# Kernel optimization log

Hardware: AMD Instinct MI355X
Metric: run time of the kernel (lower is better)

Reference implementation:

```python
import jax, jax.numpy as jnp
import numpy as np

B, S, H, NH, KVH, HD = 8, 4096, 4096, 32, 8, 128
STEP = 2048
EPS = 1e-6


def _rotate_half(x):
    x1, x2 = x[..., : HD // 2], x[..., HD // 2 :]
    return jnp.concatenate([-x2, x1], axis=-1)


def _rmsnorm(x, w):
    xf = x.astype(jnp.float32)
    var = jnp.mean(xf * xf, axis=-1, keepdims=True)
    return w * (xf * jax.lax.rsqrt(var + EPS)).astype(x.dtype)


def setup_inputs() -> dict:
    key = jax.random.key(0)
    ks = jax.random.split(key, 10)
    wscale = 0.02
    hidden_states = jax.random.normal(ks[0], (B, 1, H), jnp.float32)
    # RoPE angles for position STEP
    inv_freq = 1.0 / (10000.0 ** (jnp.arange(0, HD, 2, dtype=jnp.float32) / HD))
    ang = STEP * inv_freq  # [HD/2]
    emb = jnp.concatenate([ang, ang])  # [HD]
    cos = jnp.broadcast_to(jnp.cos(emb), (B, 1, HD)).astype(jnp.float32)
    sin = jnp.broadcast_to(jnp.sin(emb), (B, 1, HD)).astype(jnp.float32)
    key_cache = jax.random.normal(ks[1], (B, KVH, S, HD), jnp.float32)
    value_cache = jax.random.normal(ks[2], (B, KVH, S, HD), jnp.float32)
    # additive causal mask: rows 0..STEP, cols 0..S-1; -1e9 where col > row
    rows = jnp.arange(STEP + 1)[:, None]
    cols = jnp.arange(S)[None, :]
    causal_mask = jnp.where(cols <= rows, 0.0, -1e9).astype(jnp.float32)[None, None]
    q_w = jax.random.normal(ks[3], (H, NH * HD), jnp.float32) * wscale
    k_w = jax.random.normal(ks[4], (H, KVH * HD), jnp.float32) * wscale
    v_w = jax.random.normal(ks[5], (H, KVH * HD), jnp.float32) * wscale
    o_w = jax.random.normal(ks[6], (NH * HD, H), jnp.float32) * wscale
    q_norm_w = jnp.ones((HD,), jnp.float32)
    k_norm_w = jnp.ones((HD,), jnp.float32)
    return {
        "hidden_states": hidden_states, "cos": cos, "sin": sin,
        "key_cache": key_cache, "value_cache": value_cache,
        "causal_mask": causal_mask, "q_w": q_w, "k_w": k_w, "v_w": v_w,
        "o_w": o_w, "q_norm_w": q_norm_w, "k_norm_w": k_norm_w,
        "step_idx": STEP,
    }


def reference(hidden_states, cos, sin, key_cache, value_cache, causal_mask,
              q_w, k_w, v_w, o_w, q_norm_w, k_norm_w, step_idx):
    G = NH // KVH
    scaling = HD ** -0.5
    bsz = hidden_states.shape[0]
    # projections + QK-RMSNorm; (B,1,nH,HD) -> (B,nH,1,HD)
    q = _rmsnorm((hidden_states @ q_w).reshape(bsz, 1, NH, HD), q_norm_w).transpose(0, 2, 1, 3)
    k = _rmsnorm((hidden_states @ k_w).reshape(bsz, 1, KVH, HD), k_norm_w).transpose(0, 2, 1, 3)
    v = (hidden_states @ v_w).reshape(bsz, 1, KVH, HD).transpose(0, 2, 1, 3)
    # RoPE (cos/sin broadcast over head axis)
    c = cos[:, None, :, :]  # (B,1,1,HD)
    s = sin[:, None, :, :]
    q = q * c + _rotate_half(q) * s
    k = k * c + _rotate_half(k) * s
    # single-step cache write
    key_cache = key_cache.at[:, :, step_idx : step_idx + 1].set(k)
    value_cache = value_cache.at[:, :, step_idx : step_idx + 1].set(v)
    # GQA attention without materializing repeat_kv (same math)
    qg = q.reshape(bsz, KVH, G, 1, HD)
    scores = jnp.einsum("bkgqd,bksd->bkgqs", qg, key_cache) * scaling  # (B,KVH,G,1,S)
    scores = scores.reshape(bsz, NH, 1, S) + causal_mask[:, :, step_idx : step_idx + 1, :]
    attn = jax.nn.softmax(scores.astype(jnp.float32), axis=-1).astype(q.dtype)
    out = jnp.einsum("bkgqs,bksd->bkgqd", attn.reshape(bsz, KVH, G, 1, S), value_cache)
    out = out.reshape(bsz, NH, 1, HD).transpose(0, 2, 1, 3).reshape(bsz, 1, NH * HD)
    return out @ o_w
```

## Files before the change

kernel.cpp:

```cpp
#include <hip/hip_runtime.h>
#include <math.h>

#define Bq 8
#define Sq 4096
#define Hq 4096
#define NHq 32
#define KVHq 8
#define HDq 128
#define QKV_N 6144
#define CHUNK 256
#define NCHUNK 16
#define ROWS 128

__global__ __launch_bounds__(256) void gemv_splitk(
    const float* __restrict__ x, const float* __restrict__ W,
    float* __restrict__ y, int K, int ldW, int ldY) {
  int tid = threadIdx.x;
  int r0 = blockIdx.y * ROWS;
  int col = blockIdx.x * 256 + tid;
  float acc[Bq] = {0, 0, 0, 0, 0, 0, 0, 0};
  const float* wp = W + (size_t)r0 * ldW + col;
  const float* xp = x + r0;
  for (int r = 0; r < ROWS; r += 16) {
    float w[16];
#pragma unroll
    for (int j = 0; j < 16; j++) w[j] = wp[(size_t)j * ldW];
    wp += (size_t)16 * ldW;
#pragma unroll
    for (int b = 0; b < Bq; b++) {
      const float* xb = xp + b * K + r;
#pragma unroll
      for (int j = 0; j < 16; j++) acc[b] = fmaf(xb[j], w[j], acc[b]);
    }
  }
#pragma unroll
  for (int b = 0; b < Bq; b++) atomicAdd(&y[b * ldY + col], acc[b]);
}

__global__ __launch_bounds__(256) void gemv_fused_qkv(
    const float* __restrict__ x, const float* __restrict__ qw,
    const float* __restrict__ kw, const float* __restrict__ vw,
    float* __restrict__ y) {
  int tid = threadIdx.x;
  int r0 = blockIdx.y * ROWS;
  int col = blockIdx.x * 256 + tid;
  const float* W;
  int ldW, wcol;
  if (col < NHq * HDq) { W = qw; ldW = NHq * HDq; wcol = col; }
  else if (col < NHq * HDq + KVHq * HDq) { W = kw; ldW = KVHq * HDq; wcol = col - NHq * HDq; }
  else { W = vw; ldW = KVHq * HDq; wcol = col - (NHq + KVHq) * HDq; }
  float acc[Bq] = {0, 0, 0, 0, 0, 0, 0, 0};
  const float* wp = W + (size_t)r0 * ldW + wcol;
  const float* xp = x + r0;
  for (int r = 0; r < ROWS; r += 16) {
    float w[16];
#pragma unroll
    for (int j = 0; j < 16; j++) w[j] = wp[(size_t)j * ldW];
    wp += (size_t)16 * ldW;
#pragma unroll
    for (int b = 0; b < Bq; b++) {
      const float* xb = xp + b * Hq + r;
#pragma unroll
      for (int j = 0; j < 16; j++) acc[b] = fmaf(xb[j], w[j], acc[b]);
    }
  }
#pragma unroll
  for (int b = 0; b < Bq; b++) atomicAdd(&y[b * QKV_N + col], acc[b]);
}

__global__ __launch_bounds__(256) void normrope(
    const float* __restrict__ qkv, const float* __restrict__ cosp,
    const float* __restrict__ sinp, const float* __restrict__ qnw,
    const float* __restrict__ knw, const int* __restrict__ step_ptr,
    float* __restrict__ kcache, float* __restrict__ vcache,
    float* __restrict__ qvec) {
  int tid = threadIdx.x;
  int lane = tid & 63, wid = tid >> 6;
  int vec = blockIdx.x * 4 + wid;
  int step = *step_ptr;
  if (vec < 256) {
    int b = vec >> 5, h = vec & 31;
    const float* src = qkv + b * QKV_N + h * HDq;
    float x0 = src[lane], x1 = src[lane + 64];
    float ss = fmaf(x0, x0, x1 * x1);
#pragma unroll
    for (int off = 32; off; off >>= 1) ss += __shfl_xor(ss, off, 64);
    float sc = rsqrtf(ss * (1.0f / HDq) + 1e-6f);
    float n0 = x0 * sc * qnw[lane], n1 = x1 * sc * qnw[lane + 64];
    float c0 = cosp[b * HDq + lane], c1 = cosp[b * HDq + lane + 64];
    float s0 = sinp[b * HDq + lane], s1 = sinp[b * HDq + lane + 64];
    float* dst = qvec + b * (NHq * HDq) + h * HDq;
    dst[lane] = fmaf(n0, c0, -n1 * s0);
    dst[lane + 64] = fmaf(n1, c1, n0 * s1);
  } else if (vec < 320) {
    int v = vec - 256;
    int b = v >> 3, kvh = v & 7;
    const float* src = qkv + b * QKV_N + NHq * HDq + kvh * HDq;
    float x0 = src[lane], x1 = src[lane + 64];
    float ss = fmaf(x0, x0, x1 * x1);
#pragma unroll
    for (int off = 32; off; off >>= 1) ss += __shfl_xor(ss, off, 64);
    float sc = rsqrtf(ss * (1.0f / HDq) + 1e-6f);
    float n0 = x0 * sc * knw[lane], n1 = x1 * sc * knw[lane + 64];
    float c0 = cosp[b * HDq + lane], c1 = cosp[b * HDq + lane + 64];
    float s0 = sinp[b * HDq + lane], s1 = sinp[b * HDq + lane + 64];
    float* dst = kcache + (((size_t)(b * KVHq + kvh)) * Sq + step) * HDq;
    dst[lane] = fmaf(n0, c0, -n1 * s0);
    dst[lane + 64] = fmaf(n1, c1, n0 * s1);
  } else {
    int v = vec - 320;
    int b = v >> 3, kvh = v & 7;
    const float* src = qkv + b * QKV_N + (NHq + KVHq) * HDq + kvh * HDq;
    float* dst = vcache + (((size_t)(b * KVHq + kvh)) * Sq + step) * HDq;
    dst[lane] = src[lane];
    dst[lane + 64] = src[lane + 64];
  }
}

__global__ __launch_bounds__(256) void attn_partial(
    const float* __restrict__ qvec, const float* __restrict__ kc,
    const float* __restrict__ vc, const int* __restrict__ step_ptr,
    float* __restrict__ pm, float* __restrict__ pl, float* __restrict__ po) {
  int c = blockIdx.x;
  int bk = blockIdx.y;
  int b = bk >> 3, kvh = bk & 7;
  int step = *step_ptr;
  int base = c * CHUNK;
  int pidx = (bk * NCHUNK + c) * 4;
  int tid = threadIdx.x;
  if (base > step) {
    if (tid < 4) { pm[pidx + tid] = -1e38f; pl[pidx + tid] = 0.0f; }
    return;
  }
  __shared__ float qs[4][HDq];
  __shared__ float red[4][4];
  __shared__ float pls[4][CHUNK];
  __shared__ float4 ored[8][4][32];
  for (int i = tid; i < 4 * HDq; i += 256)
    qs[i >> 7][i & 127] = qvec[b * (NHq * HDq) + (kvh * 4 + (i >> 7)) * HDq + (i & 127)];
  __syncthreads();

  int s = base + tid;
  const float* krow = kc + (((size_t)bk) * Sq + s) * HDq;
  float sc[4] = {0, 0, 0, 0};
#pragma unroll 1
  for (int dd = 0; dd < HDq; dd += 32) {
    float4 kk[8];
#pragma unroll
    for (int j = 0; j < 8; j++) kk[j] = *(const float4*)(krow + dd + j * 4);
#pragma unroll
    for (int j = 0; j < 8; j++) {
#pragma unroll
      for (int g = 0; g < 4; g++) {
        float4 qq = *(const float4*)&qs[g][dd + j * 4];
        sc[g] = fmaf(kk[j].x, qq.x, sc[g]);
        sc[g] = fmaf(kk[j].y, qq.y, sc[g]);
        sc[g] = fmaf(kk[j].z, qq.z, sc[g]);
        sc[g] = fmaf(kk[j].w, qq.w, sc[g]);
      }
    }
  }
  const float scaling = 0.08838834764831845f;
  bool valid = (s <= step);
#pragma unroll
  for (int g = 0; g < 4; g++) sc[g] = valid ? sc[g] * scaling : -1e30f;

  int lane = tid & 63, wid = tid >> 6;
#pragma unroll
  for (int g = 0; g < 4; g++) {
    float v = sc[g];
#pragma unroll
    for (int off = 32; off; off >>= 1) v = fmaxf(v, __shfl_xor(v, off, 64));
    if (lane == 0) red[g][wid] = v;
  }
  __syncthreads();
  float m[4];
#pragma unroll
  for (int g = 0; g < 4; g++)
    m[g] = fmaxf(fmaxf(red[g][0], red[g][1]), fmaxf(red[g][2], red[g][3]));
  __syncthreads();
#pragma unroll
  for (int g = 0; g < 4; g++) {
    float p = __expf(sc[g] - m[g]);
    pls[g][tid] = p;
    float v = p;
#pragma unroll
    for (int off = 32; off; off >>= 1) v += __shfl_xor(v, off, 64);
    if (lane == 0) red[g][wid] = v;
  }
  __syncthreads();
  if (tid < 4) {
    pm[pidx + tid] = m[tid];
    pl[pidx + tid] = red[tid][0] + red[tid][1] + red[tid][2] + red[tid][3];
  }

  int q4 = tid & 31, grp = tid >> 5;
  const float* vb = vc + (((size_t)bk) * Sq + base + grp * 32) * HDq + q4 * 4;
  float4 o[4];
#pragma unroll
  for (int g = 0; g < 4; g++) { o[g].x = 0; o[g].y = 0; o[g].z = 0; o[g].w = 0; }
#pragma unroll 1
  for (int ss = 0; ss < 32; ss += 8) {
    float4 vv[8];
#pragma unroll
    for (int j = 0; j < 8; j++) vv[j] = *(const float4*)(vb + (size_t)(ss + j) * HDq);
#pragma unroll
    for (int j = 0; j < 8; j++) {
#pragma unroll
      for (int g = 0; g < 4; g++) {
        float p = pls[g][grp * 32 + ss + j];
        o[g].x = fmaf(p, vv[j].x, o[g].x);
        o[g].y = fmaf(p, vv[j].y, o[g].y);
        o[g].z = fmaf(p, vv[j].z, o[g].z);
        o[g].w = fmaf(p, vv[j].w, o[g].w);
      }
    }
  }
#pragma unroll
  for (int g = 0; g < 4; g++) ored[grp][g][q4] = o[g];
  __syncthreads();
  if (tid < 128) {
    int g = tid >> 5, q = tid & 31;
    float4 sum = ored[0][g][q];
#pragma unroll
    for (int r = 1; r < 8; r++) {
      float4 t = ored[r][g][q];
      sum.x += t.x; sum.y += t.y; sum.z += t.z; sum.w += t.w;
    }
    *(float4*)&po[(size_t)(pidx + g) * HDq + q * 4] = sum;
  }
}

__global__ __launch_bounds__(128) void attn_combine(
    const float* __restrict__ pm, const float* __restrict__ pl,
    const float* __restrict__ po, float* __restrict__ aout) {
  int bh = blockIdx.x;
  int b = bh >> 5, h = bh & 31;
  int kvh = h >> 2, g = h & 3;
  int d = threadIdx.x;
  int bk = b * KVHq + kvh;
  float mv[NCHUNK];
  float M = -1e38f;
#pragma unroll
  for (int c = 0; c < NCHUNK; c++) {
    mv[c] = pm[(bk * NCHUNK + c) * 4 + g];
    M = fmaxf(M, mv[c]);
  }
  float L = 0.0f, o = 0.0f;
#pragma unroll
  for (int c = 0; c < NCHUNK; c++) {
    if (mv[c] > -1e37f) {
      float w = __expf(mv[c] - M);
      L = fmaf(pl[(bk * NCHUNK + c) * 4 + g], w, L);
      o = fmaf(po[(size_t)((bk * NCHUNK + c) * 4 + g) * HDq + d], w, o);
    }
  }
  aout[b * (NHq * HDq) + h * HDq + d] = o / L;
}

extern "C" void kernel_launch(void* const* d_in, const int* in_sizes, int n_in,
                              void* d_out, int out_size, void* d_ws, size_t ws_size,
                              hipStream_t stream) {
  const float* hidden = (const float*)d_in[0];
  const float* cosp   = (const float*)d_in[1];
  const float* sinp   = (const float*)d_in[2];
  float* kcache       = (float*)d_in[3];
  float* vcache       = (float*)d_in[4];
  const float* q_w    = (const float*)d_in[6];
  const float* k_w    = (const float*)d_in[7];
  const float* v_w    = (const float*)d_in[8];
  const float* o_w    = (const float*)d_in[9];
  const float* qnw    = (const float*)d_in[10];
  const float* knw    = (const float*)d_in[11];
  const int* step_ptr = (const int*)d_in[12];
  float* out = (float*)d_out;
  float* ws = (float*)d_ws;

  float* qkv  = ws;
  float* qvec = ws + 49152;
  float* aout = ws + 81920;
  float* pm   = ws + 114688;
  float* pl   = ws + 118784;
  float* po   = ws + 122880;
  (void)in_sizes; (void)n_in; (void)ws_size;

  (void)hipMemsetAsync(qkv, 0, 49152 * sizeof(float), stream);
  (void)hipMemsetAsync(out, 0, (size_t)out_size * sizeof(float), stream);

  gemv_fused_qkv<<<dim3(QKV_N / 256, Hq / ROWS), 256, 0, stream>>>(hidden, q_w, k_w, v_w, qkv);

  normrope<<<96, 256, 0, stream>>>(qkv, cosp, sinp, qnw, knw, step_ptr, kcache, vcache, qvec);

  attn_partial<<<dim3(NCHUNK, Bq * KVHq), 256, 0, stream>>>(qvec, kcache, vcache, step_ptr, pm, pl, po);
  attn_combine<<<Bq * NHq, 128, 0, stream>>>(pm, pl, po, aout);

  gemv_splitk<<<dim3(16, Hq / ROWS), 256, 0, stream>>>(aout, o_w, out, NHq * HDq, 4096, 4096);
}
```

Measured before the change: 403.7 us.

## Replace atomic split-K GEMVs with partial buffers plus reduction, float2 weight loads

The QKV and output projection GEMVs no longer accumulate with atomicAdd into memset-cleared outputs. Each row block now writes its partial sums to a workspace slab, and a separate float4 reduction kernel sums the slabs. The memsets go away, and each thread now loads two columns of weights with float2. This removes atomic contention and memset launches but adds two extra kernels, partial-buffer traffic, and half as many blocks per GEMV.

```diff
diff --git a/kernel.cpp b/kernel.cpp
--- a/kernel.cpp
+++ b/kernel.cpp
@@ -11,61 +11,86 @@
 #define CHUNK 256
 #define NCHUNK 16
 #define ROWS 128
-
-__global__ __launch_bounds__(256) void gemv_splitk(
-    const float* __restrict__ x, const float* __restrict__ W,
-    float* __restrict__ y, int K, int ldW, int ldY) {
+#define RB 32
+
+__global__ __launch_bounds__(256) void gemv_part_qkv(
+    const float* __restrict__ x, const float* __restrict__ qw,
+    const float* __restrict__ kw, const float* __restrict__ vw,
+    float* __restrict__ part) {
   int tid = threadIdx.x;
   int r0 = blockIdx.y * ROWS;
-  int col = blockIdx.x * 256 + tid;
-  float acc[Bq] = {0, 0, 0, 0, 0, 0, 0, 0};
-  const float* wp = W + (size_t)r0 * ldW + col;
-  const float* xp = x + r0;
-  for (int r = 0; r < ROWS; r += 16) {
-    float w[16];
-#pragma unroll
-    for (int j = 0; j < 16; j++) w[j] = wp[(size_t)j * ldW];
-    wp += (size_t)16 * ldW;
-#pragma unroll
-    for (int b = 0; b < Bq; b++) {
-      const float* xb = xp + b * K + r;
-#pragma unroll
-      for (int j = 0; j < 16; j++) acc[b] = fmaf(xb[j], w[j], acc[b]);
-    }
-  }
-#pragma unroll
-  for (int b = 0; b < Bq; b++) atomicAdd(&y[b * ldY + col], acc[b]);
-}
-
-__global__ __launch_bounds__(256) void gemv_fused_qkv(
-    const float* __restrict__ x, const float* __restrict__ qw,
-    const float* __restrict__ kw, const float* __restrict__ vw,
-    float* __restrict__ y) {
-  int tid = threadIdx.x;
-  int r0 = blockIdx.y * ROWS;
-  int col = blockIdx.x * 256 + tid;
+  int col = (blockIdx.x * 256 + tid) * 2;
   const float* W;
   int ldW, wcol;
   if (col < NHq * HDq) { W = qw; ldW = NHq * HDq; wcol = col; }
   else if (col < NHq * HDq + KVHq * HDq) { W = kw; ldW = KVHq * HDq; wcol = col - NHq * HDq; }
   else { W = vw; ldW = KVHq * HDq; wcol = col - (NHq + KVHq) * HDq; }
-  float acc[Bq] = {0, 0, 0, 0, 0, 0, 0, 0};
+  float2 acc[Bq];
+#pragma unroll
+  for (int b = 0; b < Bq; b++) { acc[b].x = 0.0f; acc[b].y = 0.0f; }
   const float* wp = W + (size_t)r0 * ldW + wcol;
   const float* xp = x + r0;
   for (int r = 0; r < ROWS; r += 16) {
-    float w[16];
-#pragma unroll
-    for (int j = 0; j < 16; j++) w[j] = wp[(size_t)j * ldW];
+    float2 w[16];
+#pragma unroll
+    for (int j = 0; j < 16; j++) w[j] = *(const float2*)&wp[(size_t)j * ldW];
     wp += (size_t)16 * ldW;
 #pragma unroll
     for (int b = 0; b < Bq; b++) {
       const float* xb = xp + b * Hq + r;
 #pragma unroll
-      for (int j = 0; j < 16; j++) acc[b] = fmaf(xb[j], w[j], acc[b]);
-    }
-  }
-#pragma unroll
-  for (int b = 0; b < Bq; b++) atomicAdd(&y[b * QKV_N + col], acc[b]);
+      for (int j = 0; j < 16; j++) {
+        acc[b].x = fmaf(xb[j], w[j].x, acc[b].x);
+        acc[b].y = fmaf(xb[j], w[j].y, acc[b].y);
+      }
+    }
+  }
+  float* dst = part + (size_t)blockIdx.y * (Bq * QKV_N);
+#pragma unroll
+  for (int b = 0; b < Bq; b++) *(float2*)&dst[b * QKV_N + col] = acc[b];
+}
+
+__global__ __launch_bounds__(256) void gemv_part_o(
+    const float* __restrict__ x, const float* __restrict__ W,
+    float* __restrict__ part) {
+  int tid = threadIdx.x;
+  int r0 = blockIdx.y * ROWS;
+  int col = (blockIdx.x * 256 + tid) * 2;
+  float2 acc[Bq];
+#pragma unroll
+  for (int b = 0; b < Bq; b++) { acc[b].x = 0.0f; acc[b].y = 0.0f; }
+  const float* wp = W + (size_t)r0 * Hq + col;
+  const float* xp = x + r0;
+  for (int r = 0; r < ROWS; r += 16) {
+    float2 w[16];
+#pragma unroll
+    for (int j = 0; j < 16; j++) w[j] = *(const float2*)&wp[(size_t)j * Hq];
+    wp += (size_t)16 * Hq;
+#pragma unroll
+    for (int b = 0; b < Bq; b++) {
+      const float* xb = xp + b * Hq + r;
+#pragma unroll
+      for (int j = 0; j < 16; j++) {
+        acc[b].x = fmaf(xb[j], w[j].x, acc[b].x);
+        acc[b].y = fmaf(xb[j], w[j].y, acc[b].y);
+      }
+    }
+  }
+  float* dst = part + (size_t)blockIdx.y * (Bq * Hq);
+#pragma unroll
+  for (int b = 0; b < Bq; b++) *(float2*)&dst[b * Hq + col] = acc[b];
+}
+
+__global__ __launch_bounds__(256) void reduce_part(
+    const float* __restrict__ part, float* __restrict__ out, int n) {
+  int i = (blockIdx.x * 256 + threadIdx.x) * 4;
+  if (i >= n) return;
+  float4 s = *(const float4*)&part[i];
+  for (int rb = 1; rb < RB; rb++) {
+    float4 t = *(const float4*)&part[(size_t)rb * n + i];
+    s.x += t.x; s.y += t.y; s.z += t.z; s.w += t.w;
+  }
+  *(float4*)&out[i] = s;
 }
 
 __global__ __launch_bounds__(256) void normrope(
@@ -282,17 +307,18 @@
   float* pm   = ws + 114688;
   float* pl   = ws + 118784;
   float* po   = ws + 122880;
+  float* pq   = ws + 647168;
+  float* pout = ws + 2220032;
   (void)in_sizes; (void)n_in; (void)ws_size;
 
-  (void)hipMemsetAsync(qkv, 0, 49152 * sizeof(float), stream);
-  (void)hipMemsetAsync(out, 0, (size_t)out_size * sizeof(float), stream);
-
-  gemv_fused_qkv<<<dim3(QKV_N / 256, Hq / ROWS), 256, 0, stream>>>(hidden, q_w, k_w, v_w, qkv);
+  gemv_part_qkv<<<dim3(QKV_N / 512, RB), 256, 0, stream>>>(hidden, q_w, k_w, v_w, pq);
+  reduce_part<<<(Bq * QKV_N) / 1024, 256, 0, stream>>>(pq, qkv, Bq * QKV_N);
 
   normrope<<<96, 256, 0, stream>>>(qkv, cosp, sinp, qnw, knw, step_ptr, kcache, vcache, qvec);
 
   attn_partial<<<dim3(NCHUNK, Bq * KVHq), 256, 0, stream>>>(qvec, kcache, vcache, step_ptr, pm, pl, po);
   attn_combine<<<Bq * NHq, 128, 0, stream>>>(pm, pl, po, aout);
 
-  gemv_splitk<<<dim3(16, Hq / ROWS), 256, 0, stream>>>(aout, o_w, out, NHq * HDq, 4096, 4096);
-}
+  gemv_part_o<<<dim3(Hq / 512, RB), 256, 0, stream>>>(aout, o_w, pout);
+  reduce_part<<<(Bq * Hq) / 1024, 256, 0, stream>>>(pout, out, Bq * Hq);
+}
```

After: 412.1 us. 2.1% more time.
